# Performance work log

Hardware: AMD Instinct MI355X
Metric: run time of the kernel (lower is better)

## Reference

```python
import jax, jax.numpy as jnp
import numpy as np
from jax import lax

HID = 32  # hardcoded hid_dim in the module

def setup_inputs() -> dict:
    key = jax.random.key(0)
    ks = jax.random.split(key, 12)
    B, HIST, C, F = 512, 24, 184, 17
    PRED = 24
    IN_DIM = HIST + F  # 41
    inp = {
        "pm25_hist": jax.random.normal(ks[0], (B, HIST, C, 1), jnp.float32),
        "feature": jax.random.normal(ks[1], (B, HIST + PRED, C, F), jnp.float32),
        "time_feature": jax.random.normal(ks[2], (B, HIST + PRED, 4), jnp.float32),
        # fc_in: Linear(in_dim, 32)
        "W_in": jax.random.normal(ks[3], (HID, IN_DIM), jnp.float32) / np.sqrt(IN_DIM),
        "b_in": jnp.zeros((HID,), jnp.float32),
        # LSTMCell(32, 32): gate order i, f, g, o
        "W_ih": jax.random.normal(ks[4], (4 * HID, HID), jnp.float32) / np.sqrt(HID),
        "W_hh": jax.random.normal(ks[5], (4 * HID, HID), jnp.float32) / np.sqrt(HID),
        "b_ih": jnp.zeros((4 * HID,), jnp.float32),
        "b_hh": jnp.zeros((4 * HID,), jnp.float32),
        # fc_out: Linear(32, 1)
        "W_out": jax.random.normal(ks[6], (1, HID), jnp.float32) / np.sqrt(HID),
        "b_out": jnp.zeros((1,), jnp.float32),
    }
    return inp

def _forward(pm25_hist, feature, W_in, b_in, W_ih, W_hh, b_ih, b_hh, W_out, b_out):
    B, HIST, C, _ = pm25_hist.shape
    PRED = feature.shape[1] - HIST
    # torch: pm25_hist.reshape(B, C, -1) -- raw row-major reinterpret, same in jnp
    xn0 = pm25_hist.reshape(B, C, HIST)
    h0 = jnp.zeros((B * C, HID), pm25_hist.dtype)
    c0 = jnp.zeros((B * C, HID), pm25_hist.dtype)
    # future features, time-major for scan: [PRED, B, C, F]
    feats = jnp.moveaxis(feature[:, HIST:HIST + PRED], 1, 0)

    def step(carry, feat_t):
        xn, h, c = carry
        x = jnp.concatenate([xn, feat_t], axis=-1)          # [B, C, in_dim]
        x = x @ W_in.T + b_in                               # [B, C, HID]
        xf = x.reshape(B * C, HID)
        gates = xf @ W_ih.T + b_ih + h @ W_hh.T + b_hh      # [B*C, 4*HID]
        i, f, g, o = jnp.split(gates, 4, axis=-1)
        i = jax.nn.sigmoid(i); f = jax.nn.sigmoid(f)
        g = jnp.tanh(g);       o = jax.nn.sigmoid(o)
        c = f * c + i * g
        h = o * jnp.tanh(c)
        pred = h.reshape(B, C, HID) @ W_out.T + b_out       # [B, C, 1]
        xn = jnp.concatenate([xn[:, :, 1:], pred], axis=-1)
        return (xn, h, c), pred

    _, preds = lax.scan(step, (xn0, h0, c0), feats)
    return jnp.moveaxis(preds, 0, 1)  # [B, PRED, C, 1]

def reference(pm25_hist, feature, time_feature, W_in, b_in, W_ih, W_hh, b_ih, b_hh, W_out, b_out):
    # time_feature is accepted but unused, matching the torch module
    return _forward(pm25_hist, feature, W_in, b_in, W_ih, W_hh, b_ih, b_hh, W_out, b_out)
```

## Files before the change

### kernel.cpp

```cpp
#include <hip/hip_runtime.h>
#include <hip/hip_bf16.h>


#define BN     512
#define HISTN  24
#define CNN    184
#define FN     17
#define PREDN  24
#define HIDN   32
#define INN    41
#define CELLS  (BN * CNN)
#define FROW   (CNN * FN)
#define PMROW  (HISTN * CNN)
#define LOG2E  1.4426950408889634f

typedef __attribute__((ext_vector_type(8))) short  short8;
typedef __attribute__((ext_vector_type(4))) float  float4v;
typedef __attribute__((ext_vector_type(4))) int    int4v;

#define MFMA_B16(a, b, c) __builtin_amdgcn_mfma_f32_16x16x32_bf16(a, b, c, 0, 0, 0)

__device__ __forceinline__ short f2bf(float f) {
  union { float f; unsigned u; } v; v.f = f;
  unsigned r = v.u + 0x7fffu + ((v.u >> 16) & 1u);
  return (short)(r >> 16);
}
__device__ __forceinline__ int pack2(short lo, short hi) {
  return (int)(((unsigned)(unsigned short)lo) | (((unsigned)(unsigned short)hi) << 16));
}
__device__ __forceinline__ float sig_s(float y) {
  return __builtin_amdgcn_rcpf(1.0f + exp2f(-y));
}
__device__ __forceinline__ float tanh_s(float y) {
  const float e = exp2f(y + y);
  return 1.0f - 2.0f * __builtin_amdgcn_rcpf(1.0f + e);
}
__device__ __forceinline__ float tanh_u(float x) {
  const float e = exp2f(x * (2.0f * LOG2E));
  return 1.0f - 2.0f * __builtin_amdgcn_rcpf(1.0f + e);
}

__global__ void build_weights(const float* __restrict__ W_in, const float* __restrict__ b_in,
                              const float* __restrict__ W_ih, const float* __restrict__ W_hh,
                              const float* __restrict__ b_ih, const float* __restrict__ b_hh,
                              short* __restrict__ wfrag)
{
  const int tid = blockIdx.x * 256 + threadIdx.x;
  if (tid >= 128 * 12) return;
  const int g  = tid / 12;
  const int kg = tid % 12;
  const int k0 = kg * 8;

  float v[8];
  #pragma unroll
  for (int j = 0; j < 8; ++j) v[j] = 0.f;

  if (k0 < INN) {
    for (int m = 0; m < HIDN; ++m) {
      const float wih = W_ih[g * HIDN + m];
      #pragma unroll
      for (int j = 0; j < 8; ++j) {
        const int k = k0 + j;
        if (k < INN) v[j] += wih * W_in[m * INN + k];
      }
    }
  }
  if (k0 <= INN && INN < k0 + 8) {
    float bv = b_ih[g] + b_hh[g];
    for (int m = 0; m < HIDN; ++m) bv += W_ih[g * HIDN + m] * b_in[m];
    v[INN - k0] = bv;
  }
  if (k0 >= 64) {
    #pragma unroll
    for (int j = 0; j < 8; ++j) v[j] = W_hh[g * HIDN + (k0 + j - 64)];
  }

  const int f = kg >> 2, q = kg & 3, nt = g >> 4, c0 = g & 15;
  short* dst = wfrag + (((f * 8 + nt) * 64 + q * 16 + c0) * 8);
  #pragma unroll
  for (int j = 0; j < 8; ++j) dst[j] = f2bf(v[j] * LOG2E);
}

__global__ __launch_bounds__(256, 4)
void lstm_fused(const float* __restrict__ pm25,
                const float* __restrict__ feat,
                const short* __restrict__ wfrag,
                const float* __restrict__ W_out, const float* __restrict__ b_out,
                float* __restrict__ out)
{
  __shared__ __align__(16) short wlds[2 * 8 * 64 * 8];
  __shared__ __align__(16) short hlds[4][16][40];

  const int tid   = threadIdx.x;
  const int w     = tid >> 6;
  const int lane  = tid & 63;
  const int q     = lane >> 4;
  const int c0    = lane & 15;
  const int cell0 = blockIdx.x << 6;
  const int mycell = cell0 + (w << 4) + c0;

  {
    const int4v* src = (const int4v*)(wfrag + 8 * 64 * 8);
    int4v* dst = (int4v*)wlds;
    #pragma unroll
    for (int i = 0; i < 4; ++i) dst[tid + 256 * i] = src[tid + 256 * i];
  }

  short8 Wka[8];
  #pragma unroll
  for (int nt = 0; nt < 8; ++nt)
    Wka[nt] = *(const short8*)(wfrag + (nt * 64 + lane) * 8);

  float woutr[2];
  woutr[0] = W_out[c0]; woutr[1] = W_out[16 + c0];
  const float bo = b_out[0];

  {
    short* hz = &hlds[w][0][0];
    for (int i = lane; i < 16 * 40; i += 64) hz[i] = 0;
  }

  const int bb = mycell / CNN, cc = mycell % CNN;

  int wv[4] = {0, 0, 0, 0};
  if (q < 3) {
    const float* src = pm25 + bb * PMROW + cc * HISTN + (q << 3);
    short tmp[8];
    #pragma unroll
    for (int j = 0; j < 8; ++j) tmp[j] = f2bf(src[j]);
    #pragma unroll
    for (int i = 0; i < 4; ++i) wv[i] = pack2(tmp[2 * i], tmp[2 * i + 1]);
  }

  const int pfo = (q == 3) ? 0 : (q == 0) ? 8 : 16;
  const float* fptr = feat + (size_t)(bb * 48 + HISTN) * FROW + cc * FN + pfo;
  float pf[8] = {0.f, 0.f, 0.f, 0.f, 0.f, 0.f, 0.f, 0.f};
  if (q != 2) {
    if (q == 1) pf[0] = fptr[0];
    else {
      #pragma unroll
      for (int i = 0; i < 8; ++i) pf[i] = fptr[i];
    }
  }

  int obase[4];
  #pragma unroll
  for (int r = 0; r < 4; ++r) {
    const int cgr = cell0 + (w << 4) + (q << 2) + r;
    obase[r] = (cgr / CNN) * (PREDN * CNN) + (cgr % CNN);
  }

  float cst[2][4] = {{0.f, 0.f, 0.f, 0.f}, {0.f, 0.f, 0.f, 0.f}};

  __syncthreads();

  const char* wl = (const char*)wlds;
  int wbase = lane * 16;
  const short* hrd = &hlds[w][c0][q << 3];
  short* hw = &hlds[w][0][0];

  union WU { int i[4]; short8 v8; };

  #pragma unroll 1
  for (int t = 0; t < PREDN; ++t) {
    asm volatile("" : "+v"(wbase));

    WU au;
    au.i[0] = wv[0]; au.i[1] = wv[1]; au.i[2] = wv[2]; au.i[3] = wv[3];
    if (q == 3) {
      #pragma unroll
      for (int i = 0; i < 4; ++i) au.i[i] = pack2(f2bf(pf[2 * i]), f2bf(pf[2 * i + 1]));
    }
    const short8 ka = au.v8;

    WU bu;
    bu.i[0] = 0; bu.i[1] = 0; bu.i[2] = 0; bu.i[3] = 0;
    if (q == 0) {
      #pragma unroll
      for (int i = 0; i < 4; ++i) bu.i[i] = pack2(f2bf(pf[2 * i]), f2bf(pf[2 * i + 1]));
    } else if (q == 1) {
      bu.i[0] = pack2(f2bf(pf[0]), (short)0x3f80);
    }
    const short8 kb = bu.v8;

    const short8 kc = *(const short8*)hrd;

    if (t < PREDN - 1 && q != 2) {
      fptr += FROW;
      if (q == 1) pf[0] = fptr[0];
      else {
        #pragma unroll
        for (int i = 0; i < 8; ++i) pf[i] = fptr[i];
      }
    }

    __builtin_amdgcn_s_setprio(1);
    const float4v z4 = {0.f, 0.f, 0.f, 0.f};
    float4v acc[8];
    #pragma unroll
    for (int nt = 0; nt < 8; ++nt) {
      float4v a = MFMA_B16(ka, Wka[nt], z4);
      const short8 wkb = *(const short8*)(wl + wbase + nt * 1024);
      a = MFMA_B16(kb, wkb, a);
      const short8 wkc = *(const short8*)(wl + wbase + 8192 + nt * 1024);
      a = MFMA_B16(kc, wkc, a);
      acc[nt] = a;
    }
    __builtin_amdgcn_s_setprio(0);

    float part[4] = {0.f, 0.f, 0.f, 0.f};
    #pragma unroll
    for (int s = 0; s < 2; ++s) {
      #pragma unroll
      for (int r = 0; r < 4; ++r) {
        const float iv = sig_s(acc[0 + s][r]);
        const float fv = sig_s(acc[2 + s][r]);
        const float gv = tanh_s(acc[4 + s][r]);
        const float ov = sig_s(acc[6 + s][r]);
        const float cn = fv * cst[s][r] + iv * gv;
        cst[s][r] = cn;
        const float hv = ov * tanh_u(cn);
        hw[((q << 2) + r) * 40 + (s << 4) + c0] = f2bf(hv);
        part[r] += woutr[s] * hv;
      }
    }

    #pragma unroll
    for (int r = 0; r < 4; ++r) {
      float p = part[r];
      p += __shfl_xor(p, 1);
      p += __shfl_xor(p, 2);
      p += __shfl_xor(p, 4);
      p += __shfl_xor(p, 8);
      part[r] = p;
    }
    if (c0 == 0) {
      #pragma unroll
      for (int r = 0; r < 4; ++r)
        out[obase[r] + t * CNN] = part[r] + bo;
    }

    if (t < PREDN - 1) {
      const float v01 = (c0 & 1) ? part[1] : part[0];
      const float v23 = (c0 & 1) ? part[3] : part[2];
      const float vs  = (c0 & 2) ? v23 : v01;
      const float pv = __shfl(vs, ((c0 >> 2) << 4) | c0) + bo;
      const int pw = (int)(unsigned short)f2bf(pv);
      const int nb = __shfl(wv[0], (lane + 16) & 63);
      const int inc = (q == 2) ? pw : nb;
      wv[0] = (int)(((unsigned)wv[0] >> 16) | ((unsigned)wv[1] << 16));
      wv[1] = (int)(((unsigned)wv[1] >> 16) | ((unsigned)wv[2] << 16));
      wv[2] = (int)(((unsigned)wv[2] >> 16) | ((unsigned)wv[3] << 16));
      wv[3] = (int)(((unsigned)wv[3] >> 16) | ((unsigned)inc   << 16));
    }
  }
}

extern "C" void kernel_launch(void* const* d_in, const int* in_sizes, int n_in,
                              void* d_out, int out_size, void* d_ws, size_t ws_size,
                              hipStream_t stream) {
  (void)in_sizes; (void)n_in; (void)out_size; (void)ws_size;
  const float* pm25  = (const float*)d_in[0];
  const float* feat  = (const float*)d_in[1];
  const float* W_in  = (const float*)d_in[3];
  const float* b_in  = (const float*)d_in[4];
  const float* W_ih  = (const float*)d_in[5];
  const float* W_hh  = (const float*)d_in[6];
  const float* b_ih  = (const float*)d_in[7];
  const float* b_hh  = (const float*)d_in[8];
  const float* W_out = (const float*)d_in[9];
  const float* b_out = (const float*)d_in[10];
  float* out = (float*)d_out;

  short* wfrag = (short*)d_ws;

  build_weights<<<dim3(6), dim3(256), 0, stream>>>(
      W_in, b_in, W_ih, W_hh, b_ih, b_hh, wfrag);
  lstm_fused<<<dim3(CELLS / 64), dim3(256), 0, stream>>>(
      pm25, feat, wfrag, W_out, b_out, out);
}
```

Baseline: 535.5 us.

## Pair reciprocals in gate activations, read kb/kc weights from global, use packed bf16 converts

Gate columns are permuted so each lane holds hidden units 2*c0 and 2*c0+1, which lets it write one packed bf16 pair per row. Sigmoid and tanh now share one reciprocal per pair of exponentials, cutting the number of v_rcp per step. The tanh scale for the g gate is folded into the weights. The LDS staging of the kb/kc weight fragments and the block barrier are removed; those fragments are read straight from global/L2 each step. Input packing uses v_cvt_pk_bf16_f32 and is hoisted out of the MFMA critical path. The paired reciprocal can lose accuracy or overflow when exponentials are large, and the global weight reads depend on cache hits.

```diff
diff --git a/kernel.cpp b/kernel.cpp
--- a/kernel.cpp
+++ b/kernel.cpp
@@ -1,5 +1,4 @@
 #include <hip/hip_runtime.h>
-#include <hip/hip_bf16.h>
 
 
 #define BN     512
@@ -16,28 +15,26 @@
 
 typedef __attribute__((ext_vector_type(8))) short  short8;
 typedef __attribute__((ext_vector_type(4))) float  float4v;
-typedef __attribute__((ext_vector_type(4))) int    int4v;
-
-#define MFMA_B16(a, b, c) __builtin_amdgcn_mfma_f32_16x16x32_bf16(a, b, c, 0, 0, 0)
+
+#define MFMA_B16(a,b,c) __builtin_amdgcn_mfma_f32_16x16x32_bf16(a,b,c,0,0,0)
+#define X2(x) __builtin_amdgcn_exp2f(x)
 
 __device__ __forceinline__ short f2bf(float f) {
   union { float f; unsigned u; } v; v.f = f;
   unsigned r = v.u + 0x7fffu + ((v.u >> 16) & 1u);
   return (short)(r >> 16);
 }
-__device__ __forceinline__ int pack2(short lo, short hi) {
-  return (int)(((unsigned)(unsigned short)lo) | (((unsigned)(unsigned short)hi) << 16));
-}
-__device__ __forceinline__ float sig_s(float y) {
-  return __builtin_amdgcn_rcpf(1.0f + exp2f(-y));
-}
-__device__ __forceinline__ float tanh_s(float y) {
-  const float e = exp2f(y + y);
-  return 1.0f - 2.0f * __builtin_amdgcn_rcpf(1.0f + e);
-}
-__device__ __forceinline__ float tanh_u(float x) {
-  const float e = exp2f(x * (2.0f * LOG2E));
-  return 1.0f - 2.0f * __builtin_amdgcn_rcpf(1.0f + e);
+__device__ __forceinline__ int cvt_pk_bf16(float lo, float hi) {
+  int r;
+  asm("v_cvt_pk_bf16_f32 %0, %1, %2" : "=v"(r) : "v"(lo), "v"(hi));
+  return r;
+}
+__device__ __forceinline__ void rcp_pair(float ea, float eb, float& ra, float& rb) {
+  const float s  = ea + eb;
+  const float p  = fmaf(ea, eb, s) + 1.0f;
+  const float rr = __builtin_amdgcn_rcpf(p);
+  ra = fmaf(eb, rr, rr);
+  rb = fmaf(ea, rr, rr);
 }
 
 __global__ void build_weights(const float* __restrict__ W_in, const float* __restrict__ b_in,
@@ -75,10 +72,15 @@
     for (int j = 0; j < 8; ++j) v[j] = W_hh[g * HIDN + (k0 + j - 64)];
   }
 
-  const int f = kg >> 2, q = kg & 3, nt = g >> 4, c0 = g & 15;
+  const int tau = g >> 5;
+  const int jj  = g & 31;
+  const int nt  = tau * 2 + (jj & 1);
+  const int c0  = jj >> 1;
+  const int f   = kg >> 2, q = kg & 3;
+  const float scale = (tau == 2) ? (2.0f * LOG2E) : LOG2E;
   short* dst = wfrag + (((f * 8 + nt) * 64 + q * 16 + c0) * 8);
   #pragma unroll
-  for (int j = 0; j < 8; ++j) dst[j] = f2bf(v[j] * LOG2E);
+  for (int j = 0; j < 8; ++j) dst[j] = f2bf(v[j] * scale);
 }
 
 __global__ __launch_bounds__(256, 4)
@@ -88,7 +90,6 @@
                 const float* __restrict__ W_out, const float* __restrict__ b_out,
                 float* __restrict__ out)
 {
-  __shared__ __align__(16) short wlds[2 * 8 * 64 * 8];
   __shared__ __align__(16) short hlds[4][16][40];
 
   const int tid   = threadIdx.x;
@@ -99,20 +100,13 @@
   const int cell0 = blockIdx.x << 6;
   const int mycell = cell0 + (w << 4) + c0;
 
-  {
-    const int4v* src = (const int4v*)(wfrag + 8 * 64 * 8);
-    int4v* dst = (int4v*)wlds;
-    #pragma unroll
-    for (int i = 0; i < 4; ++i) dst[tid + 256 * i] = src[tid + 256 * i];
-  }
-
   short8 Wka[8];
   #pragma unroll
   for (int nt = 0; nt < 8; ++nt)
     Wka[nt] = *(const short8*)(wfrag + (nt * 64 + lane) * 8);
 
-  float woutr[2];
-  woutr[0] = W_out[c0]; woutr[1] = W_out[16 + c0];
+  const float woutr0 = W_out[2 * c0];
+  const float woutr1 = W_out[2 * c0 + 1];
   const float bo = b_out[0];
 
   {
@@ -129,19 +123,24 @@
     #pragma unroll
     for (int j = 0; j < 8; ++j) tmp[j] = f2bf(src[j]);
     #pragma unroll
-    for (int i = 0; i < 4; ++i) wv[i] = pack2(tmp[2 * i], tmp[2 * i + 1]);
+    for (int i = 0; i < 4; ++i)
+      wv[i] = (int)(((unsigned)(unsigned short)tmp[2 * i]) |
+                    (((unsigned)(unsigned short)tmp[2 * i + 1]) << 16));
   }
 
   const int pfo = (q == 3) ? 0 : (q == 0) ? 8 : 16;
   const float* fptr = feat + (size_t)(bb * 48 + HISTN) * FROW + cc * FN + pfo;
-  float pf[8] = {0.f, 0.f, 0.f, 0.f, 0.f, 0.f, 0.f, 0.f};
-  if (q != 2) {
-    if (q == 1) pf[0] = fptr[0];
-    else {
-      #pragma unroll
-      for (int i = 0; i < 8; ++i) pf[i] = fptr[i];
-    }
-  }
+  float pf[8];
+  #pragma unroll
+  for (int i = 0; i < 8; ++i) pf[i] = 0.f;
+  if (q == 1) { pf[0] = fptr[0]; pf[1] = 1.0f; }
+  else if (q != 2) {
+    #pragma unroll
+    for (int i = 0; i < 8; ++i) pf[i] = fptr[i];
+  }
+  int ci[4];
+  #pragma unroll
+  for (int i = 0; i < 4; ++i) ci[i] = cvt_pk_bf16(pf[2 * i], pf[2 * i + 1]);
 
   int obase[4];
   #pragma unroll
@@ -150,45 +149,35 @@
     obase[r] = (cgr / CNN) * (PREDN * CNN) + (cgr % CNN);
   }
 
-  float cst[2][4] = {{0.f, 0.f, 0.f, 0.f}, {0.f, 0.f, 0.f, 0.f}};
-
-  __syncthreads();
-
-  const char* wl = (const char*)wlds;
-  int wbase = lane * 16;
+  float cst0[4] = {0.f, 0.f, 0.f, 0.f};
+  float cst1[4] = {0.f, 0.f, 0.f, 0.f};
+
+  const char* wkb = (const char*)wfrag + 8192;
+  int wofs = lane * 16;
   const short* hrd = &hlds[w][c0][q << 3];
-  short* hw = &hlds[w][0][0];
 
   union WU { int i[4]; short8 v8; };
 
   #pragma unroll 1
   for (int t = 0; t < PREDN; ++t) {
-    asm volatile("" : "+v"(wbase));
-
-    WU au;
-    au.i[0] = wv[0]; au.i[1] = wv[1]; au.i[2] = wv[2]; au.i[3] = wv[3];
-    if (q == 3) {
-      #pragma unroll
-      for (int i = 0; i < 4; ++i) au.i[i] = pack2(f2bf(pf[2 * i]), f2bf(pf[2 * i + 1]));
-    }
+    asm volatile("" : "+v"(wofs));
+
+    WU au, bu;
+    #pragma unroll
+    for (int i = 0; i < 4; ++i) au.i[i] = (q == 3) ? ci[i] : wv[i];
+    bu.i[0] = (q < 2)  ? ci[0] : 0;
+    bu.i[1] = (q == 0) ? ci[1] : 0;
+    bu.i[2] = (q == 0) ? ci[2] : 0;
+    bu.i[3] = (q == 0) ? ci[3] : 0;
     const short8 ka = au.v8;
-
-    WU bu;
-    bu.i[0] = 0; bu.i[1] = 0; bu.i[2] = 0; bu.i[3] = 0;
-    if (q == 0) {
-      #pragma unroll
-      for (int i = 0; i < 4; ++i) bu.i[i] = pack2(f2bf(pf[2 * i]), f2bf(pf[2 * i + 1]));
-    } else if (q == 1) {
-      bu.i[0] = pack2(f2bf(pf[0]), (short)0x3f80);
-    }
     const short8 kb = bu.v8;
-
     const short8 kc = *(const short8*)hrd;
 
-    if (t < PREDN - 1 && q != 2) {
+    const bool pfv = (t < PREDN - 1);
+    if (pfv) {
       fptr += FROW;
       if (q == 1) pf[0] = fptr[0];
-      else {
+      else if (q != 2) {
         #pragma unroll
         for (int i = 0; i < 8; ++i) pf[i] = fptr[i];
       }
@@ -200,29 +189,45 @@
     #pragma unroll
     for (int nt = 0; nt < 8; ++nt) {
       float4v a = MFMA_B16(ka, Wka[nt], z4);
-      const short8 wkb = *(const short8*)(wl + wbase + nt * 1024);
-      a = MFMA_B16(kb, wkb, a);
-      const short8 wkc = *(const short8*)(wl + wbase + 8192 + nt * 1024);
-      a = MFMA_B16(kc, wkc, a);
+      const short8 wb = *(const short8*)(wkb + wofs + nt * 1024);
+      a = MFMA_B16(kb, wb, a);
+      const short8 wc = *(const short8*)(wkb + 8192 + wofs + nt * 1024);
+      a = MFMA_B16(kc, wc, a);
       acc[nt] = a;
     }
     __builtin_amdgcn_s_setprio(0);
 
     float part[4] = {0.f, 0.f, 0.f, 0.f};
     #pragma unroll
-    for (int s = 0; s < 2; ++s) {
+    for (int r = 0; r < 4; ++r) {
+      const float ei0 = X2(-acc[0][r]), ei1 = X2(-acc[1][r]);
+      const float ef0 = X2(-acc[2][r]), ef1 = X2(-acc[3][r]);
+      const float eg0 = X2( acc[4][r]), eg1 = X2( acc[5][r]);
+      const float eo0 = X2(-acc[6][r]), eo1 = X2(-acc[7][r]);
+      float si0, sf0, si1, sf1, rg0, so0, rg1, so1;
+      rcp_pair(ei0, ef0, si0, sf0);
+      rcp_pair(ei1, ef1, si1, sf1);
+      rcp_pair(eg0, eo0, rg0, so0);
+      rcp_pair(eg1, eo1, rg1, so1);
+      const float tg0 = fmaf(-2.f, rg0, 1.f);
+      const float tg1 = fmaf(-2.f, rg1, 1.f);
+      const float cn0 = fmaf(sf0, cst0[r], si0 * tg0);
+      const float cn1 = fmaf(sf1, cst1[r], si1 * tg1);
+      cst0[r] = cn0; cst1[r] = cn1;
+      const float ec0 = X2(cn0 * (2.f * LOG2E));
+      const float ec1 = X2(cn1 * (2.f * LOG2E));
+      float rc0, rc1;
+      rcp_pair(ec0, ec1, rc0, rc1);
+      const float h0 = so0 * fmaf(-2.f, rc0, 1.f);
+      const float h1 = so1 * fmaf(-2.f, rc1, 1.f);
+      *(int*)&hlds[w][(q << 2) + r][c0 << 1] = cvt_pk_bf16(h0, h1);
+      part[r] = fmaf(woutr0, h0, part[r]);
+      part[r] = fmaf(woutr1, h1, part[r]);
+    }
+
+    if (pfv) {
       #pragma unroll
-      for (int r = 0; r < 4; ++r) {
-        const float iv = sig_s(acc[0 + s][r]);
-        const float fv = sig_s(acc[2 + s][r]);
-        const float gv = tanh_s(acc[4 + s][r]);
-        const float ov = sig_s(acc[6 + s][r]);
-        const float cn = fv * cst[s][r] + iv * gv;
-        cst[s][r] = cn;
-        const float hv = ov * tanh_u(cn);
-        hw[((q << 2) + r) * 40 + (s << 4) + c0] = f2bf(hv);
-        part[r] += woutr[s] * hv;
-      }
+      for (int i = 0; i < 4; ++i) ci[i] = cvt_pk_bf16(pf[2 * i], pf[2 * i + 1]);
     }
 
     #pragma unroll
@@ -240,7 +245,7 @@
         out[obase[r] + t * CNN] = part[r] + bo;
     }
 
-    if (t < PREDN - 1) {
+    if (pfv) {
       const float v01 = (c0 & 1) ? part[1] : part[0];
       const float v23 = (c0 & 1) ? part[3] : part[2];
       const float vs  = (c0 & 2) ? v23 : v01;
```

Result: slower. 569.4 us (+6.3%).
